# Performance work log

Measured on AMD Instinct MI355X. Metric: run time of the kernel, lower is better.

Reference implementation:

```python
import jax, jax.numpy as jnp
import numpy as np

B, N = 2, 2048
D_MODEL, HEADS = 512, 8
D_K = D_MODEL // HEADS
D_HIDDEN = 2048
MIN_SPREAD = 2.0
MIN_RBF = 1e-3
MAX_RBF = 1.0
LN_EPS = 1e-5


def setup_inputs() -> dict:
    key = jax.random.key(0)
    ks = jax.random.split(key, 12)
    xs = (6.0 / (D_K + D_MODEL)) ** 0.5
    q = jax.random.normal(ks[0], (B, N, D_MODEL), dtype=jnp.float32)
    k = jax.random.normal(ks[1], (B, N, D_MODEL), dtype=jnp.float32)
    v = jax.random.normal(ks[2], (B, N, D_MODEL), dtype=jnp.float32)
    coords = jax.random.normal(ks[3], (B, N, 3), dtype=jnp.float32) * 10.0
    mask = jnp.ones((B, N), dtype=bool)
    q_proj = jax.random.uniform(ks[4], (HEADS, D_MODEL, D_K), minval=-xs, maxval=xs)
    k_proj = jax.random.uniform(ks[5], (HEADS, D_MODEL, D_K), minval=-xs, maxval=xs)
    v_proj = jax.random.uniform(ks[6], (HEADS, D_MODEL, D_K), minval=-xs, maxval=xs)
    q_bias = jnp.zeros((HEADS, D_K))
    k_bias = jnp.zeros((HEADS, D_K))
    v_bias = jnp.zeros((HEADS, D_K))
    ow = (1.0 / D_MODEL) ** 0.5
    out_w = jax.random.uniform(ks[7], (D_MODEL, D_MODEL), minval=-ow, maxval=ow)
    spread_w = jnp.zeros((HEADS,))
    beta_w = jnp.zeros((HEADS,))
    ln1_g = jnp.ones((D_MODEL,)); ln1_b = jnp.zeros((D_MODEL,))
    ln2_g = jnp.ones((D_MODEL,)); ln2_b = jnp.zeros((D_MODEL,))
    w1 = jax.random.normal(ks[8], (D_MODEL, D_HIDDEN)) * 0.02
    b1 = jnp.zeros((D_HIDDEN,))
    w2 = jax.random.normal(ks[9], (D_HIDDEN, D_MODEL)) * 0.02
    b2 = jnp.zeros((D_MODEL,))
    return dict(q=q, k=k, v=v, coords=coords, mask=mask,
                q_proj=q_proj, k_proj=k_proj, v_proj=v_proj,
                q_bias=q_bias, k_bias=k_bias, v_bias=v_bias,
                out_w=out_w, spread_w=spread_w, beta_w=beta_w,
                ln1_g=ln1_g, ln1_b=ln1_b, ln2_g=ln2_g, ln2_b=ln2_b,
                w1=w1, b1=b1, w2=w2, b2=b2)


def _layernorm(x, g, b):
    mu = jnp.mean(x, axis=-1, keepdims=True)
    var = jnp.mean((x - mu) ** 2, axis=-1, keepdims=True)
    return (x - mu) * jax.lax.rsqrt(var + LN_EPS) * g + b


def _geo_attention(q, k, v, coords, mask,
                   q_proj, k_proj, v_proj, q_bias, k_bias, v_bias,
                   out_w, spread_w, beta_w):
    # per-head projections: [B,H,N,dk]
    Q = jnp.einsum('bnd,hdk->bhnk', q, q_proj) + q_bias[None, :, None, :]
    K = jnp.einsum('bnd,hdk->bhnk', k, k_proj) + k_bias[None, :, None, :]
    V = jnp.einsum('bnd,hdk->bhnk', v, v_proj) + v_bias[None, :, None, :]

    spreads = MIN_SPREAD + jnp.exp(spread_w)   # [H]
    betas = jnp.exp(beta_w)                    # [H]

    # pairwise squared distances [B,N,N]
    d2 = jnp.sum((coords[:, :, None, :] - coords[:, None, :, :]) ** 2, axis=-1)
    # per-head Gaussian RBF [B,H,N,N]
    rbf = jnp.exp(-d2[:, None, :, :] / (2.0 * spreads[None, :, None, None] ** 2))

    scores = jnp.einsum('bhnk,bhmk->bhnm', Q, K) / jnp.sqrt(jnp.float32(D_K))
    scores = betas[None, :, None, None] * rbf * scores

    # sparsity: keys with rbf outside [min_rbf, max_rbf] or padded are masked out
    valid = (rbf >= MIN_RBF) & (rbf <= MAX_RBF) & mask[:, None, None, :]
    scores = jnp.where(valid, scores, -jnp.inf)
    attn = jax.nn.softmax(scores, axis=-1)     # diagonal always valid (rbf=1)

    out = jnp.einsum('bhnm,bhmk->bhnk', attn, V)         # [B,H,N,dk]
    # torch: out.permute(0,2,3,1).reshape(B,N,d_model) -> (b,n,dk,h) layout
    out = jnp.transpose(out, (0, 2, 3, 1)).reshape(out.shape[0], out.shape[2], D_MODEL)
    return out @ out_w.T


def reference(q, k, v, coords, mask,
              q_proj, k_proj, v_proj, q_bias, k_bias, v_bias,
              out_w, spread_w, beta_w,
              ln1_g, ln1_b, ln2_g, ln2_b, w1, b1, w2, b2):
    attn_out = _geo_attention(q, k, v, coords, mask,
                              q_proj, k_proj, v_proj, q_bias, k_bias, v_bias,
                              out_w, spread_w, beta_w)
    x = _layernorm(q + attn_out, ln1_g, ln1_b)
    ffn = jax.nn.relu(x @ w1 + b1) @ w2 + b2
    x = _layernorm(x + ffn, ln2_g, ln2_b)
    return x
```

## Files before the change

kernel.cpp:

```cpp
#include <hip/hip_runtime.h>
#include <math.h>

typedef __attribute__((ext_vector_type(8))) short bf16x8;
typedef __attribute__((ext_vector_type(4))) float f32x4;

#define MFMA16(a,b,c) __builtin_amdgcn_mfma_f32_16x16x32_bf16((a),(b),(c),0,0,0)
#define LOG2E 1.44269504f

__device__ __forceinline__ unsigned short f2bf(float f) {
    union { float f; unsigned u; } x; x.f = f;
    unsigned r = x.u + 0x7FFFu + ((x.u >> 16) & 1u);
    return (unsigned short)(r >> 16);
}

__device__ __forceinline__ unsigned cvt_pk_bf16(float lo, float hi) {
    unsigned r;
    asm("v_cvt_pk_bf16_f32 %0, %1, %2" : "=v"(r) : "v"(lo), "v"(hi));
    return r;
}

__device__ __forceinline__ float exp2_fast(float x) {
    float r; asm("v_exp_f32 %0, %1" : "=v"(r) : "v"(x)); return r;
}

__global__ __launch_bounds__(256) void transpose_w(
    const float* __restrict__ in, unsigned short* __restrict__ outb, int R, int C)
{
    __shared__ float t[32][33];
    const int tx = threadIdx.x & 31, ty = threadIdx.x >> 5;
    const int c0 = blockIdx.x << 5, r0 = blockIdx.y << 5;
#pragma unroll
    for (int i = 0; i < 4; ++i)
        t[ty + i * 8][tx] = in[(long)(r0 + ty + i * 8) * C + c0 + tx];
    __syncthreads();
#pragma unroll
    for (int i = 0; i < 4; ++i)
        outb[(long)(c0 + ty + i * 8) * R + r0 + tx] = f2bf(t[tx][ty + i * 8]);
}

__global__ __launch_bounds__(256) void cvt_weights(
    const float* __restrict__ qp, const float* __restrict__ kp,
    const float* __restrict__ vp, const float* __restrict__ ow,
    const float* __restrict__ qbias, const float* __restrict__ kbias,
    const float* __restrict__ vbias,
    unsigned short* __restrict__ qpT, unsigned short* __restrict__ kpT,
    unsigned short* __restrict__ vpT, unsigned short* __restrict__ owT,
    float* __restrict__ biasC)
{
    const int NP = 262144;
    const int total = 4 * NP + 1536;
    for (int i = blockIdx.x * 256 + threadIdx.x; i < total; i += gridDim.x * 256) {
        if (i < 3 * NP) {
            int which = i / NP, r = i - which * NP;
            int n = r >> 9, d = r & 511;
            int h = n >> 6, kk = n & 63;
            const float* src = (which == 0) ? qp : (which == 1) ? kp : vp;
            unsigned short* dst = (which == 0) ? qpT : (which == 1) ? kpT : vpT;
            dst[r] = f2bf(src[(h << 15) + (d << 6) + kk]);
        } else if (i < 4 * NP) {
            int r = i - 3 * NP;
            int oi = r >> 9, f = r & 511;
            int h = f >> 6, kk = f & 63;
            owT[r] = f2bf(ow[(oi << 9) + (kk << 3) + h]);
        } else {
            int j = i - 4 * NP;
            biasC[j] = (j < 512) ? qbias[j] : (j < 1024) ? kbias[j - 512] : vbias[j - 1024];
        }
    }
}

template<int TM, int BNT, int AF32, int RELU, int SF32, int SB16, int SVTR, int SQKV>
__global__ __launch_bounds__(256) void gemm_bt(
    const void* __restrict__ Aq,
    const void* __restrict__ Ak,
    const void* __restrict__ Av,
    const unsigned short* __restrict__ Bt,
    const float* __restrict__ bias,
    float* __restrict__ Cf, unsigned short* __restrict__ Cb,
    unsigned short* __restrict__ Cb2, unsigned short* __restrict__ Cb3,
    int M, int N, int K)
{
    constexpr int MI = TM / 32;
    constexpr int BC = BNT / 32;
    __shared__ unsigned short As[TM][72];
    __shared__ unsigned short Bs[BNT][72];
    const int tid = threadIdx.x;
    const int m0 = blockIdx.y * TM, n0 = blockIdx.x * BNT;
    const int wv = tid >> 6, lane = tid & 63;
    const int lrow = lane & 15, kg = lane >> 4;
    const int wr = (wv >> 1) * (TM / 2), wc = (wv & 1) * (BNT / 2);

    const void* A = Aq;
    if (SQKV) A = (n0 < 512) ? Aq : (n0 < 1024) ? Ak : Av;

    f32x4 acc[MI][BC];
    const f32x4 z4 = {0.f, 0.f, 0.f, 0.f};
#pragma unroll
    for (int i = 0; i < MI; ++i)
#pragma unroll
        for (int j = 0; j < BC; ++j) acc[i][j] = z4;

    const int nkt = K >> 6;
    for (int kt = 0; kt < nkt; ++kt) {
        __syncthreads();
        const int k0 = kt << 6;
#pragma unroll
        for (int i = 0; i < MI; ++i) {
            int slot = tid + (i << 8);
            int r = slot >> 3, c = (slot & 7) << 3;
            if (AF32) {
                const float* Af = (const float*)A;
                float4 a0 = *(const float4*)(&Af[(long)(m0 + r) * K + k0 + c]);
                float4 a1 = *(const float4*)(&Af[(long)(m0 + r) * K + k0 + c + 4]);
                int4 w;
                w.x = (int)cvt_pk_bf16(a0.x, a0.y);
                w.y = (int)cvt_pk_bf16(a0.z, a0.w);
                w.z = (int)cvt_pk_bf16(a1.x, a1.y);
                w.w = (int)cvt_pk_bf16(a1.z, a1.w);
                *(int4*)(&As[r][c]) = w;
            } else {
                const unsigned short* Ab = (const unsigned short*)A;
                *(int4*)(&As[r][c]) = *(const int4*)(&Ab[(long)(m0 + r) * K + k0 + c]);
            }
        }
#pragma unroll
        for (int i = 0; i < BC; ++i) {
            int slot = tid + (i << 8);
            int r = slot >> 3, c = (slot & 7) << 3;
            *(int4*)(&Bs[r][c]) = *(const int4*)(&Bt[(long)(n0 + r) * K + k0 + c]);
        }
        __syncthreads();
#pragma unroll
        for (int ks = 0; ks < 2; ++ks) {
            const int koff = (ks << 5) + (kg << 3);
            bf16x8 af[MI], bfr[BC];
#pragma unroll
            for (int mi = 0; mi < MI; ++mi)
                af[mi] = *(const bf16x8*)(&As[wr + (mi << 4) + lrow][koff]);
#pragma unroll
            for (int ni = 0; ni < BC; ++ni)
                bfr[ni] = *(const bf16x8*)(&Bs[wc + (ni << 4) + lrow][koff]);
#pragma unroll
            for (int mi = 0; mi < MI; ++mi)
#pragma unroll
                for (int ni = 0; ni < BC; ++ni)
                    acc[mi][ni] = MFMA16(af[mi], bfr[ni], acc[mi][ni]);
        }
    }

#pragma unroll
    for (int mi = 0; mi < MI; ++mi) {
#pragma unroll
        for (int ni = 0; ni < BC; ++ni) {
            const int col = n0 + wc + (ni << 4) + lrow;
            const float bv = bias ? bias[col] : 0.0f;
#pragma unroll
            for (int j = 0; j < 4; ++j) {
                const int row = m0 + wr + (mi << 4) + (kg << 2) + j;
                float val = acc[mi][ni][j] + bv;
                if (RELU) val = fmaxf(val, 0.0f);
                if (SF32) Cf[(long)row * N + col] = val;
                if (SB16) Cb[(long)row * N + col] = f2bf(val);
                if (SVTR)
                    Cb[((long)(row >> 11) << 20) + ((long)col << 11) + (row & 2047)] = f2bf(val);
                if (SQKV) {
                    if (n0 < 512)
                        Cb[(long)row * 512 + col] = f2bf(val);
                    else if (n0 < 1024)
                        Cb2[(long)row * 512 + (col - 512)] = f2bf(val);
                    else {
                        const int c2 = col - 1024;
                        Cb3[((long)(row >> 11) << 20) + ((long)c2 << 11) + (row & 2047)] = f2bf(val);
                    }
                }
            }
        }
    }
}

__global__ __launch_bounds__(256) void geo_attn(
    const unsigned short* __restrict__ Qh,
    const unsigned short* __restrict__ Kh,
    const unsigned short* __restrict__ VhT,
    const float* __restrict__ coords,
    const float* __restrict__ spread_w, const float* __restrict__ beta_w,
    unsigned short* __restrict__ Ob)
{
    __shared__ unsigned short Ks[64][72];
    __shared__ unsigned short Vs[64][72];
    __shared__ unsigned short Ps[4][16][72];
    __shared__ float4 ck4[64];

    const int tid = threadIdx.x;
    const int bid = blockIdx.x;
    const int swz = ((bid & 7) << 6) + (bid >> 3);
    const int bh = swz >> 5, qt = swz & 31;
    const int b = bh >> 3, h = bh & 7;
    const int wv = tid >> 6, lane = tid & 63;
    const int lq = lane & 15, kg = lane >> 4;
    const float NEG_INF = -__builtin_inff();
    const float THRL = 8.0f * LOG2E;
    const float RCUT = -9.96578428f;

    const float spread = 2.0f + __expf(spread_w[h]);
    const float inv2s2l = LOG2E / (2.0f * spread * spread);
    const float coefL = __expf(beta_w[h]) * 0.125f * LOG2E;

    const long qrow = (long)(b * 2048 + qt * 64 + (wv << 4) + lq);
    const bf16x8 qA = *(const bf16x8*)(&Qh[qrow * 512 + h * 64 + (kg << 3)]);
    const bf16x8 qB = *(const bf16x8*)(&Qh[qrow * 512 + h * 64 + 32 + (kg << 3)]);

    float cqx, cqy, cqz;
    {
        long ca = qrow * 3;
        cqx = coords[ca]; cqy = coords[ca + 1]; cqz = coords[ca + 2];
    }

    float mrun = NEG_INF, lrun = 0.0f;
    f32x4 Oa[4];
    const f32x4 z4 = {0.f, 0.f, 0.f, 0.f};
#pragma unroll
    for (int nd = 0; nd < 4; ++nd) Oa[nd] = z4;

    const long kbase0 = ((long)b * 2048) * 512 + h * 64;
    const long vbase = ((long)(b * 8 + h)) * 131072;

    for (int kt = 0; kt < 32; ++kt) {
        __syncthreads();
        const int k0 = kt << 6;
#pragma unroll
        for (int i = 0; i < 2; ++i) {
            int slot = tid + (i << 8);
            int r = slot >> 3, c = (slot & 7) << 3;
            *(int4*)(&Ks[r][c]) = *(const int4*)(&Kh[kbase0 + (long)(k0 + r) * 512 + c]);
            *(int4*)(&Vs[r][c]) = *(const int4*)(&VhT[vbase + (long)r * 2048 + k0 + c]);
        }
        if (tid < 64) {
            long ca = ((long)(b * 2048 + k0 + tid)) * 3;
            ck4[tid] = make_float4(coords[ca], coords[ca + 1], coords[ca + 2], 0.0f);
        }
        __syncthreads();

        f32x4 t4[4];
#pragma unroll
        for (int ra = 0; ra < 4; ++ra) t4[ra] = z4;
#pragma unroll
        for (int ks = 0; ks < 2; ++ks) {
            const int koff = (ks << 5) + (kg << 3);
            const bf16x8 bq = ks ? qB : qA;
#pragma unroll
            for (int ra = 0; ra < 4; ++ra) {
                bf16x8 ak = *(const bf16x8*)(&Ks[(ra << 4) + lq][koff]);
                t4[ra] = MFMA16(ak, bq, t4[ra]);
            }
        }

        float tmax = NEG_INF;
#pragma unroll
        for (int ra = 0; ra < 4; ++ra) {
#pragma unroll
            for (int j = 0; j < 4; ++j) {
                float4 ck = ck4[(ra << 4) + (kg << 2) + j];
                float dx = cqx - ck.x, dy = cqy - ck.y, dz = cqz - ck.z;
                float d2 = dx * dx + dy * dy + dz * dz;
                float rexp = -d2 * inv2s2l;
                float rbf = exp2_fast(rexp);
                float val = (rexp >= RCUT) ? coefL * rbf * t4[ra][j] : NEG_INF;
                t4[ra][j] = val;
                tmax = fmaxf(tmax, val);
            }
        }
        tmax = fmaxf(tmax, __shfl_xor(tmax, 16, 64));
        tmax = fmaxf(tmax, __shfl_xor(tmax, 32, 64));

        const bool grow_any = __any(tmax > mrun + THRL);
        float psum = 0.0f;
        if (grow_any) {
            const float mn = fmaxf(mrun, tmax);
            const bool dead = (mn == NEG_INF);
            const float meff = dead ? 0.0f : mn;
            const float fcorr = dead ? 1.0f : exp2_fast(mrun - mn);
#pragma unroll
            for (int ra = 0; ra < 4; ++ra)
#pragma unroll
                for (int j = 0; j < 4; ++j) {
                    float p = exp2_fast(t4[ra][j] - meff);
                    t4[ra][j] = p;
                    psum += p;
                }
            psum += __shfl_xor(psum, 16, 64);
            psum += __shfl_xor(psum, 32, 64);
            mrun = mn;
            lrun = lrun * fcorr + psum;
            float fb[4];
#pragma unroll
            for (int j = 0; j < 4; ++j)
                fb[j] = __shfl(fcorr, (lane & 48) | ((kg << 2) + j), 64);
#pragma unroll
            for (int nd = 0; nd < 4; ++nd)
#pragma unroll
                for (int j = 0; j < 4; ++j)
                    Oa[nd][j] *= fb[j];
        } else {
            const float meff = (mrun == NEG_INF) ? 0.0f : mrun;
#pragma unroll
            for (int ra = 0; ra < 4; ++ra)
#pragma unroll
                for (int j = 0; j < 4; ++j) {
                    float p = exp2_fast(t4[ra][j] - meff);
                    t4[ra][j] = p;
                    psum += p;
                }
            psum += __shfl_xor(psum, 16, 64);
            psum += __shfl_xor(psum, 32, 64);
            lrun += psum;
        }

#pragma unroll
        for (int ra = 0; ra < 4; ++ra) {
            uint2 pk;
            pk.x = cvt_pk_bf16(t4[ra][0], t4[ra][1]);
            pk.y = cvt_pk_bf16(t4[ra][2], t4[ra][3]);
            *(uint2*)(&Ps[wv][lq][(ra << 4) + (kg << 2)]) = pk;
        }

#pragma unroll
        for (int ks = 0; ks < 2; ++ks) {
            const int koff = (ks << 5) + (kg << 3);
            bf16x8 ap = *(const bf16x8*)(&Ps[wv][lq][koff]);
#pragma unroll
            for (int nd = 0; nd < 4; ++nd) {
                bf16x8 bv = *(const bf16x8*)(&Vs[(nd << 4) + lq][koff]);
                Oa[nd] = MFMA16(ap, bv, Oa[nd]);
            }
        }
    }

    const float inv = 1.0f / lrun;
    float il[4];
#pragma unroll
    for (int j = 0; j < 4; ++j)
        il[j] = __shfl(inv, (lane & 48) | ((kg << 2) + j), 64);
    const long obase = ((long)(b * 2048 + qt * 64 + (wv << 4))) * 512 + h * 64;
#pragma unroll
    for (int nd = 0; nd < 4; ++nd)
#pragma unroll
        for (int j = 0; j < 4; ++j)
            Ob[obase + (long)((kg << 2) + j) * 512 + (nd << 4) + lq] =
                f2bf(Oa[nd][j] * il[j]);
}

template<int SB16>
__global__ __launch_bounds__(256) void ln_res(
    const float* __restrict__ X, const float* __restrict__ R,
    const float* __restrict__ g, const float* __restrict__ bb,
    float* __restrict__ Yf, unsigned short* __restrict__ Yb)
{
    const int wv = threadIdx.x >> 6, lane = threadIdx.x & 63;
    const long row = (long)blockIdx.x * 4 + wv;
    const float* xp = X + row * 512;
    const float* rp = R + row * 512;
    const int c0 = lane * 8;
    float4 a0 = *(const float4*)(xp + c0);
    float4 a1 = *(const float4*)(xp + c0 + 4);
    float4 r0 = *(const float4*)(rp + c0);
    float4 r1 = *(const float4*)(rp + c0 + 4);
    float v[8] = {a0.x + r0.x, a0.y + r0.y, a0.z + r0.z, a0.w + r0.w,
                  a1.x + r1.x, a1.y + r1.y, a1.z + r1.z, a1.w + r1.w};
    float s = 0.f, ss = 0.f;
#pragma unroll
    for (int i = 0; i < 8; ++i) { s += v[i]; ss += v[i] * v[i]; }
#pragma unroll
    for (int off = 1; off < 64; off <<= 1) {
        s += __shfl_xor(s, off, 64);
        ss += __shfl_xor(ss, off, 64);
    }
    const float mu = s * (1.0f / 512.0f);
    const float var = ss * (1.0f / 512.0f) - mu * mu;
    const float rstd = rsqrtf(var + 1e-5f);
#pragma unroll
    for (int i = 0; i < 8; ++i) {
        const int c = c0 + i;
        const float y = (v[i] - mu) * rstd * g[c] + bb[c];
        Yf[row * 512 + c] = y;
        if (SB16) Yb[row * 512 + c] = f2bf(y);
    }
}

extern "C" void kernel_launch(void* const* d_in, const int* in_sizes, int n_in,
                              void* d_out, int out_size, void* d_ws, size_t ws_size,
                              hipStream_t stream)
{
    const float* q      = (const float*)d_in[0];
    const float* k      = (const float*)d_in[1];
    const float* v      = (const float*)d_in[2];
    const float* coords = (const float*)d_in[3];
    const float* q_proj = (const float*)d_in[5];
    const float* k_proj = (const float*)d_in[6];
    const float* v_proj = (const float*)d_in[7];
    const float* q_bias = (const float*)d_in[8];
    const float* k_bias = (const float*)d_in[9];
    const float* v_bias = (const float*)d_in[10];
    const float* out_w  = (const float*)d_in[11];
    const float* spread_w = (const float*)d_in[12];
    const float* beta_w = (const float*)d_in[13];
    const float* ln1_g  = (const float*)d_in[14];
    const float* ln1_b  = (const float*)d_in[15];
    const float* ln2_g  = (const float*)d_in[16];
    const float* ln2_b  = (const float*)d_in[17];
    const float* w1     = (const float*)d_in[18];
    const float* b1     = (const float*)d_in[19];
    const float* w2     = (const float*)d_in[20];
    const float* b2     = (const float*)d_in[21];
    float* out = (float*)d_out;

    char* ws = (char*)d_ws;
    size_t off = 0;
    auto alloc = [&](size_t bytes) -> void* {
        void* p = ws + off;
        off += (bytes + 255) & ~(size_t)255;
        return p;
    };
    unsigned short* qpT  = (unsigned short*)alloc(512UL * 512 * 2);
    unsigned short* kpT  = (unsigned short*)alloc(512UL * 512 * 2);
    unsigned short* vpT  = (unsigned short*)alloc(512UL * 512 * 2);
    unsigned short* owT  = (unsigned short*)alloc(512UL * 512 * 2);
    unsigned short* w1T  = (unsigned short*)alloc(2048UL * 512 * 2);
    unsigned short* w2T  = (unsigned short*)alloc(512UL * 2048 * 2);
    float* biasC = (float*)alloc(1536UL * 4);
    unsigned short* Qp   = (unsigned short*)alloc(4096UL * 512 * 2);
    unsigned short* Kp   = (unsigned short*)alloc(4096UL * 512 * 2);
    unsigned short* VpT  = (unsigned short*)alloc(4096UL * 512 * 2);
    unsigned short* attnb= (unsigned short*)alloc(4096UL * 512 * 2);
    float* proj = (float*)alloc(4096UL * 512 * 4);
    float* x1   = (float*)alloc(4096UL * 512 * 4);
    unsigned short* x1b = (unsigned short*)alloc(4096UL * 512 * 2);
    unsigned short* hid = (unsigned short*)alloc(4096UL * 2048 * 2);
    float* ffn  = (float*)alloc(4096UL * 512 * 4);
    (void)ws_size; (void)in_sizes; (void)n_in; (void)out_size;

    cvt_weights<<<2048, 256, 0, stream>>>(q_proj, k_proj, v_proj, out_w,
                                          q_bias, k_bias, v_bias,
                                          qpT, kpT, vpT, owT, biasC);
    transpose_w<<<dim3(64, 16), 256, 0, stream>>>(w1, w1T, 512, 2048);
    transpose_w<<<dim3(16, 64), 256, 0, stream>>>(w2, w2T, 2048, 512);

    gemm_bt<128, 128, 1, 0, 0, 0, 0, 1><<<dim3(12, 32), 256, 0, stream>>>(
        q, k, v, qpT, biasC, nullptr, Qp, Kp, VpT, 4096, 1536, 512);

    geo_attn<<<512, 256, 0, stream>>>(Qp, Kp, VpT, coords, spread_w, beta_w, attnb);

    gemm_bt<128, 64, 0, 0, 1, 0, 0, 0><<<dim3(8, 32), 256, 0, stream>>>(
        attnb, nullptr, nullptr, owT, nullptr, proj, nullptr, nullptr, nullptr, 4096, 512, 512);
    ln_res<1><<<1024, 256, 0, stream>>>(proj, q, ln1_g, ln1_b, x1, x1b);

    gemm_bt<128, 128, 0, 1, 0, 1, 0, 0><<<dim3(16, 32), 256, 0, stream>>>(
        x1b, nullptr, nullptr, w1T, b1, nullptr, hid, nullptr, nullptr, 4096, 2048, 512);
    gemm_bt<128, 64, 0, 0, 1, 0, 0, 0><<<dim3(8, 32), 256, 0, stream>>>(
        hid, nullptr, nullptr, w2T, b2, ffn, nullptr, nullptr, nullptr, 4096, 512, 2048);
    ln_res<0><<<1024, 256, 0, stream>>>(ffn, x1, ln2_g, ln2_b, out, nullptr);
}
```

Before: 195.6 us.

## Split-K the output-projection and FFN-down GEMMs, reducing the partials in layernorm

The two GEMMs with N=512 (the attention output projection and the second FFN matmul) now run with a 2-way split over K via blockIdx.z. Each half writes an fp32 partial, and only the first half adds the bias. The residual layernorm kernel gains an optional second input and sums both partials before normalizing. This doubles the block count of these launches to fill the device better, at the cost of extra fp32 partial traffic. The second partial buffers alias the hid and proj workspaces, relying on launch ordering for safety.

```diff
diff --git a/kernel.cpp b/kernel.cpp
--- a/kernel.cpp
+++ b/kernel.cpp
@@ -69,14 +69,15 @@
     }
 }
 
-template<int TM, int BNT, int AF32, int RELU, int SF32, int SB16, int SVTR, int SQKV>
+template<int TM, int BNT, int AF32, int RELU, int SF32, int SB16, int SVTR, int SQKV, int SPLITK>
 __global__ __launch_bounds__(256) void gemm_bt(
     const void* __restrict__ Aq,
     const void* __restrict__ Ak,
     const void* __restrict__ Av,
     const unsigned short* __restrict__ Bt,
     const float* __restrict__ bias,
-    float* __restrict__ Cf, unsigned short* __restrict__ Cb,
+    float* __restrict__ Cf, float* __restrict__ Cf2,
+    unsigned short* __restrict__ Cb,
     unsigned short* __restrict__ Cb2, unsigned short* __restrict__ Cb3,
     int M, int N, int K)
 {
@@ -89,9 +90,11 @@
     const int wv = tid >> 6, lane = tid & 63;
     const int lrow = lane & 15, kg = lane >> 4;
     const int wr = (wv >> 1) * (TM / 2), wc = (wv & 1) * (BNT / 2);
+    const int kb = SPLITK ? blockIdx.z : 0;
 
     const void* A = Aq;
     if (SQKV) A = (n0 < 512) ? Aq : (n0 < 1024) ? Ak : Av;
+    float* Cfo = (SPLITK && kb) ? Cf2 : Cf;
 
     f32x4 acc[MI][BC];
     const f32x4 z4 = {0.f, 0.f, 0.f, 0.f};
@@ -101,7 +104,9 @@
         for (int j = 0; j < BC; ++j) acc[i][j] = z4;
 
     const int nkt = K >> 6;
-    for (int kt = 0; kt < nkt; ++kt) {
+    const int kt0 = SPLITK ? kb * (nkt >> 1) : 0;
+    const int kt1 = SPLITK ? kt0 + (nkt >> 1) : nkt;
+    for (int kt = kt0; kt < kt1; ++kt) {
         __syncthreads();
         const int k0 = kt << 6;
 #pragma unroll
@@ -153,13 +158,13 @@
 #pragma unroll
         for (int ni = 0; ni < BC; ++ni) {
             const int col = n0 + wc + (ni << 4) + lrow;
-            const float bv = bias ? bias[col] : 0.0f;
+            const float bv = (bias && kb == 0) ? bias[col] : 0.0f;
 #pragma unroll
             for (int j = 0; j < 4; ++j) {
                 const int row = m0 + wr + (mi << 4) + (kg << 2) + j;
                 float val = acc[mi][ni][j] + bv;
                 if (RELU) val = fmaxf(val, 0.0f);
-                if (SF32) Cf[(long)row * N + col] = val;
+                if (SF32) Cfo[(long)row * N + col] = val;
                 if (SB16) Cb[(long)row * N + col] = f2bf(val);
                 if (SVTR)
                     Cb[((long)(row >> 11) << 20) + ((long)col << 11) + (row & 2047)] = f2bf(val);
@@ -352,7 +357,8 @@
 
 template<int SB16>
 __global__ __launch_bounds__(256) void ln_res(
-    const float* __restrict__ X, const float* __restrict__ R,
+    const float* __restrict__ X, const float* __restrict__ X2,
+    const float* __restrict__ R,
     const float* __restrict__ g, const float* __restrict__ bb,
     float* __restrict__ Yf, unsigned short* __restrict__ Yb)
 {
@@ -367,6 +373,13 @@
     float4 r1 = *(const float4*)(rp + c0 + 4);
     float v[8] = {a0.x + r0.x, a0.y + r0.y, a0.z + r0.z, a0.w + r0.w,
                   a1.x + r1.x, a1.y + r1.y, a1.z + r1.z, a1.w + r1.w};
+    if (X2) {
+        const float* x2p = X2 + row * 512;
+        float4 b0 = *(const float4*)(x2p + c0);
+        float4 b1 = *(const float4*)(x2p + c0 + 4);
+        v[0] += b0.x; v[1] += b0.y; v[2] += b0.z; v[3] += b0.w;
+        v[4] += b1.x; v[5] += b1.y; v[6] += b1.z; v[7] += b1.w;
+    }
     float s = 0.f, ss = 0.f;
 #pragma unroll
     for (int i = 0; i < 8; ++i) { s += v[i]; ss += v[i] * v[i]; }
@@ -437,6 +450,8 @@
     unsigned short* x1b = (unsigned short*)alloc(4096UL * 512 * 2);
     unsigned short* hid = (unsigned short*)alloc(4096UL * 2048 * 2);
     float* ffn  = (float*)alloc(4096UL * 512 * 4);
+    float* proj1 = (float*)hid;
+    float* ffn1  = (float*)proj;
     (void)ws_size; (void)in_sizes; (void)n_in; (void)out_size;
 
     cvt_weights<<<2048, 256, 0, stream>>>(q_proj, k_proj, v_proj, out_w,
@@ -445,18 +460,21 @@
     transpose_w<<<dim3(64, 16), 256, 0, stream>>>(w1, w1T, 512, 2048);
     transpose_w<<<dim3(16, 64), 256, 0, stream>>>(w2, w2T, 2048, 512);
 
-    gemm_bt<128, 128, 1, 0, 0, 0, 0, 1><<<dim3(12, 32), 256, 0, stream>>>(
-        q, k, v, qpT, biasC, nullptr, Qp, Kp, VpT, 4096, 1536, 512);
+    gemm_bt<128, 128, 1, 0, 0, 0, 0, 1, 0><<<dim3(12, 32), 256, 0, stream>>>(
+        q, k, v, qpT, biasC, nullptr, nullptr, Qp, Kp, VpT, 4096, 1536, 512);
 
     geo_attn<<<512, 256, 0, stream>>>(Qp, Kp, VpT, coords, spread_w, beta_w, attnb);
 
-    gemm_bt<128, 64, 0, 0, 1, 0, 0, 0><<<dim3(8, 32), 256, 0, stream>>>(
-        attnb, nullptr, nullptr, owT, nullptr, proj, nullptr, nullptr, nullptr, 4096, 512, 512);
-    ln_res<1><<<1024, 256, 0, stream>>>(proj, q, ln1_g, ln1_b, x1, x1b);
-
-    gemm_bt<128, 128, 0, 1, 0, 1, 0, 0><<<dim3(16, 32), 256, 0, stream>>>(
-        x1b, nullptr, nullptr, w1T, b1, nullptr, hid, nullptr, nullptr, 4096, 2048, 512);
-    gemm_bt<128, 64, 0, 0, 1, 0, 0, 0><<<dim3(8, 32), 256, 0, stream>>>(
-        hid, nullptr, nullptr, w2T, b2, ffn, nullptr, nullptr, nullptr, 4096, 512, 2048);
-    ln_res<0><<<1024, 256, 0, stream>>>(ffn, x1, ln2_g, ln2_b, out, nullptr);
-}
+    gemm_bt<128, 64, 0, 0, 1, 0, 0, 0, 1><<<dim3(8, 32, 2), 256, 0, stream>>>(
+        attnb, nullptr, nullptr, owT, nullptr, proj, proj1, nullptr, nullptr, nullptr,
+        4096, 512, 512);
+    ln_res<1><<<1024, 256, 0, stream>>>(proj, proj1, q, ln1_g, ln1_b, x1, x1b);
+
+    gemm_bt<128, 128, 0, 1, 0, 1, 0, 0, 0><<<dim3(16, 32), 256, 0, stream>>>(
+        x1b, nullptr, nullptr, w1T, b1, nullptr, nullptr, hid, nullptr, nullptr,
+        4096, 2048, 512);
+    gemm_bt<128, 64, 0, 0, 1, 0, 0, 0, 1><<<dim3(8, 32, 2), 256, 0, stream>>>(
+        hid, nullptr, nullptr, w2T, b2, ffn, ffn1, nullptr, nullptr, nullptr,
+        4096, 512, 2048);
+    ln_res<0><<<1024, 256, 0, stream>>>(ffn, ffn1, x1, ln2_g, ln2_b, out, nullptr);
+}
```

Result: faster. 189.2 us (median of 2 runs) (-3.3%).
